# Kernel tuning notes

Measured on AMD Instinct MI355X. Metric: run time of the kernel, lower is better.

## Reference

```python
import jax, jax.numpy as jnp
import numpy as np

N, E, IN_C, HEADS, OUT_C = 50000, 800000, 256, 8, 32
NEG_SLOPE = 0.2
BN_EPS = 1e-5


def setup_inputs() -> dict:
    key = jax.random.key(0)
    ks = jax.random.split(key, 12)
    x = jax.random.normal(ks[0], (N, IN_C), jnp.float32)
    edge_index = jax.random.randint(ks[1], (2, E), 0, N, dtype=jnp.int32)
    edge_attr = jax.random.uniform(ks[2], (E, 1), jnp.float32)
    s = 0.1
    W = jax.random.normal(ks[3], (IN_C, HEADS * OUT_C), jnp.float32) * s
    att_src = jax.random.normal(ks[4], (HEADS, OUT_C), jnp.float32) * s
    att_dst = jax.random.normal(ks[5], (HEADS, OUT_C), jnp.float32) * s
    W_edge = jax.random.normal(ks[6], (1, HEADS * OUT_C), jnp.float32) * s
    att_edge = jax.random.normal(ks[7], (HEADS, OUT_C), jnp.float32) * s
    bias = jnp.zeros((HEADS * OUT_C,), jnp.float32)
    gamma = jnp.ones((HEADS * OUT_C,), jnp.float32)
    beta = jnp.zeros((HEADS * OUT_C,), jnp.float32)
    return {"x": x, "edge_index": edge_index, "edge_attr": edge_attr, "W": W,
            "att_src": att_src, "att_dst": att_dst, "W_edge": W_edge,
            "att_edge": att_edge, "bias": bias, "gamma": gamma, "beta": beta}


def reference(x, edge_index, edge_attr, W, att_src, att_dst, W_edge, att_edge, bias, gamma, beta):
    # --- add self loops (fill_value='mean' for edge_attr, PyG GATConv default) ---
    loops = jnp.arange(N, dtype=edge_index.dtype)
    src = jnp.concatenate([edge_index[0], loops])      # [E+N]
    dst = jnp.concatenate([edge_index[1], loops])      # [E+N]
    ea_mean = jnp.mean(edge_attr, axis=0, keepdims=True)
    ea = jnp.concatenate([edge_attr, jnp.broadcast_to(ea_mean, (N, edge_attr.shape[1]))], axis=0)

    # --- linear projections ---
    h = (x @ W).reshape(N, HEADS, OUT_C)               # [N,H,C]
    a_src = jnp.einsum('nhc,hc->nh', h, att_src)       # [N,H]
    a_dst = jnp.einsum('nhc,hc->nh', h, att_dst)       # [N,H]
    he = (ea @ W_edge).reshape(-1, HEADS, OUT_C)       # [E+N,H,C]
    a_edge = jnp.einsum('ehc,hc->eh', he, att_edge)    # [E+N,H]

    # --- edge-wise attention logits + segment softmax over destination nodes ---
    alpha = jax.nn.leaky_relu(a_src[src] + a_dst[dst] + a_edge, NEG_SLOPE)  # [E+N,H]
    amax = jax.ops.segment_max(alpha, dst, num_segments=N)  # every node has a self loop
    alpha = jnp.exp(alpha - amax[dst])
    asum = jax.ops.segment_sum(alpha, dst, num_segments=N)
    alpha = alpha / (asum[dst] + 1e-16)

    # --- weighted aggregation (attention dropout is identity in eval) ---
    msg = alpha[:, :, None] * h[src]                   # [E+N,H,C]
    out = jax.ops.segment_sum(msg, dst, num_segments=N).reshape(N, HEADS * OUT_C) + bias

    # --- BatchNorm (batch stats) + ELU; feature dropout is identity in eval ---
    mean = jnp.mean(out, axis=0)
    var = jnp.var(out, axis=0)
    out = (out - mean) * jax.lax.rsqrt(var + BN_EPS) * gamma + beta
    return jax.nn.elu(out)
```

## Files before the change

kernel.cpp:

```cpp
#include <hip/hip_runtime.h>
#include <hip/hip_bf16.h>
#include <math.h>

#define HEADS 8
#define OUTC 32
#define INC 256
#define OC 256
#define NEG_SLOPE 0.2f
#define BN_EPS 1e-5f
#define HS_STRIDE 264

typedef __attribute__((ext_vector_type(8))) short short8;
typedef __attribute__((ext_vector_type(4))) float floatx4;

__device__ __forceinline__ float bf2f(ushort u) {
    union { uint i; float f; } c; c.i = ((uint)u) << 16; return c.f;
}
__device__ __forceinline__ ushort f2bf(float f) {
    union { float f; uint i; } c; c.f = f;
    uint i = c.i + 0x7fffu + ((c.i >> 16) & 1u);
    return (ushort)(i >> 16);
}
__device__ __forceinline__ float loadf(const void* src, int t, uint flag) {
    return flag ? bf2f(((const ushort*)src)[t]) : ((const float*)src)[t];
}
__device__ __forceinline__ uint dtype_flag(const uint* gamma_raw) {
    return gamma_raw[0] != 0x3F800000u ? 1u : 0u;
}

__global__ void k_setup(const void* __restrict__ W, ushort* __restrict__ WT,
                        const void* __restrict__ att_src, const void* __restrict__ att_dst,
                        const void* __restrict__ gamma, const void* __restrict__ beta,
                        const void* __restrict__ We, const void* __restrict__ ae,
                        float* __restrict__ attS, float* __restrict__ attD,
                        float* __restrict__ gam, float* __restrict__ bet,
                        float* __restrict__ cvals, float* __restrict__ stats,
                        const void* __restrict__ eattr, const int* __restrict__ ei,
                        float* __restrict__ easum, int* __restrict__ deg, int E) {
    uint flag = dtype_flag((const uint*)gamma);
    int b = blockIdx.x, t = threadIdx.x;
    if (b < 256) {
        float v = loadf(W, b * OC + t, flag);
        WT[(size_t)t * INC + b] = f2bf(v);
    } else if (b == 256) {
        attS[t] = loadf(att_src, t, flag);
        attD[t] = loadf(att_dst, t, flag);
        gam[t]  = loadf(gamma, t, flag);
        bet[t]  = loadf(beta, t, flag);
        stats[t] = 0.f;
        stats[OC + t] = 0.f;
        __shared__ float s[OC];
        s[t] = loadf(We, t, flag) * loadf(ae, t, flag);
        __syncthreads();
        if (t < HEADS) {
            float v = 0.f;
            #pragma unroll
            for (int j = 0; j < OUTC; j++) v += s[t * OUTC + j];
            cvals[t] = v;
        }
    } else {
        int eb = b - 257;
        float v = 0.f;
        for (int i = eb * 256 + t; i < E; i += 512 * 256) {
            v += loadf(eattr, i, flag);
            atomicAdd(&deg[ei[E + i]], 1);
        }
        #pragma unroll
        for (int off = 32; off; off >>= 1) v += __shfl_down(v, off, 64);
        if ((t & 63) == 0) atomicAdd(easum, v);
    }
}

__global__ void __launch_bounds__(256, 2) k_gemm(const void* __restrict__ xraw,
                                                 const ushort* __restrict__ WT,
                                                 ushort* __restrict__ Hb,
                                                 const float* __restrict__ attS,
                                                 const float* __restrict__ attD,
                                                 float* __restrict__ asrc,
                                                 float* __restrict__ adst,
                                                 int N, const uint* __restrict__ graw) {
    uint flag = dtype_flag(graw);
    __shared__ ushort hs[16 * HS_STRIDE];
    int wave = threadIdx.x >> 6;
    int lane = threadIdx.x & 63;
    int m = lane & 15, q = lane >> 4;

    short8 bfr[4][8];
    #pragma unroll
    for (int i = 0; i < 4; i++) {
        const short8* wb = (const short8*)(WT + (size_t)((wave * 4 + i) * 16 + m) * INC);
        #pragma unroll
        for (int kk = 0; kk < 8; kk++) bfr[i][kk] = wb[kk * 4 + q];
    }

    int row0 = blockIdx.x << 4;
    #pragma unroll
    for (int c = 0; c < 2; c++) {
        int ch = threadIdx.x * 2 + c;
        int r = ch >> 5, seg = ch & 31;
        int row = row0 + r; if (row > N - 1) row = N - 1;
        short8 v;
        if (flag) {
            v = *(const short8*)((const ushort*)xraw + (size_t)row * INC + seg * 8);
        } else {
            const float4* xf = (const float4*)((const float*)xraw + (size_t)row * INC + seg * 8);
            float4 f0 = xf[0], f1 = xf[1];
            v[0] = (short)f2bf(f0.x); v[1] = (short)f2bf(f0.y);
            v[2] = (short)f2bf(f0.z); v[3] = (short)f2bf(f0.w);
            v[4] = (short)f2bf(f1.x); v[5] = (short)f2bf(f1.y);
            v[6] = (short)f2bf(f1.z); v[7] = (short)f2bf(f1.w);
        }
        *(short8*)(hs + r * HS_STRIDE + seg * 8) = v;
    }
    __syncthreads();
    short8 afr[8];
    #pragma unroll
    for (int kk = 0; kk < 8; kk++)
        afr[kk] = *(const short8*)(hs + m * HS_STRIDE + kk * 32 + q * 8);
    __syncthreads();
    floatx4 acc[4];
    #pragma unroll
    for (int i = 0; i < 4; i++) {
        floatx4 a = {0.f, 0.f, 0.f, 0.f};
        #pragma unroll
        for (int kk = 0; kk < 8; kk++)
            a = __builtin_amdgcn_mfma_f32_16x16x32_bf16(afr[kk], bfr[i][kk], a, 0, 0, 0);
        acc[i] = a;
    }
    #pragma unroll
    for (int i = 0; i < 4; i++) {
        int col = (wave * 4 + i) * 16 + m;
        #pragma unroll
        for (int r4 = 0; r4 < 4; r4++)
            hs[(q * 4 + r4) * HS_STRIDE + col] = f2bf(acc[i][r4]);
    }
    __syncthreads();
    #pragma unroll
    for (int c = 0; c < 2; c++) {
        int ch = threadIdx.x * 2 + c;
        int r = ch >> 5, seg = ch & 31;
        int row = row0 + r;
        if (row < N) {
            short8 v = *(const short8*)(hs + r * HS_STRIDE + seg * 8);
            *(short8*)(Hb + (size_t)row * OC + seg * 8) = v;
        }
    }
    if (threadIdx.x < 128) {
        int lr = threadIdx.x >> 3, hd = threadIdx.x & 7;
        int n = row0 + lr;
        if (n < N) {
            const ushort4* hrow = (const ushort4*)(hs + lr * HS_STRIDE + hd * OUTC);
            const float* as = attS + hd * OUTC;
            const float* ad = attD + hd * OUTC;
            float s1 = 0.f, s2 = 0.f;
            #pragma unroll
            for (int c4 = 0; c4 < 8; c4++) {
                ushort4 u = hrow[c4];
                float v0 = bf2f(u.x), v1 = bf2f(u.y), v2 = bf2f(u.z), v3 = bf2f(u.w);
                s1 += v0 * as[c4*4+0] + v1 * as[c4*4+1] + v2 * as[c4*4+2] + v3 * as[c4*4+3];
                s2 += v0 * ad[c4*4+0] + v1 * ad[c4*4+1] + v2 * ad[c4*4+2] + v3 * ad[c4*4+3];
            }
            asrc[n * HEADS + hd] = s1;
            adst[n * HEADS + hd] = s2;
        }
    }
}

__global__ void k_scan_local(const int* __restrict__ deg, int* __restrict__ part,
                             int* __restrict__ bsum, int N) {
    __shared__ int sth[256];
    int b = blockIdx.x, t = threadIdx.x;
    int base = b * 1024 + t * 4;
    int v0 = 0, v1 = 0, v2 = 0, v3 = 0;
    if (base + 0 < N) v0 = deg[base + 0] + 1;
    if (base + 1 < N) v1 = deg[base + 1] + 1;
    if (base + 2 < N) v2 = deg[base + 2] + 1;
    if (base + 3 < N) v3 = deg[base + 3] + 1;
    int tsum = v0 + v1 + v2 + v3;
    sth[t] = tsum;
    __syncthreads();
    #pragma unroll
    for (int off = 1; off < 256; off <<= 1) {
        int x = (t >= off) ? sth[t - off] : 0;
        __syncthreads();
        sth[t] += x;
        __syncthreads();
    }
    int excl = sth[t] - tsum;
    if (base + 0 < N) part[base + 0] = excl;
    if (base + 1 < N) part[base + 1] = excl + v0;
    if (base + 2 < N) part[base + 2] = excl + v0 + v1;
    if (base + 3 < N) part[base + 3] = excl + v0 + v1 + v2;
    if (t == 255) bsum[b] = sth[255];
}

__global__ void k_scan_blocks(const int* __restrict__ bsum, int* __restrict__ boff,
                              int nb, int* __restrict__ total) {
    __shared__ int sdata[256];
    __shared__ int carry;
    int t = threadIdx.x;
    if (t == 0) carry = 0;
    __syncthreads();
    for (int base = 0; base < nb; base += 256) {
        int v = (base + t < nb) ? bsum[base + t] : 0;
        sdata[t] = v;
        __syncthreads();
        #pragma unroll
        for (int off = 1; off < 256; off <<= 1) {
            int x = (t >= off) ? sdata[t - off] : 0;
            __syncthreads();
            sdata[t] += x;
            __syncthreads();
        }
        if (base + t < nb) boff[base + t] = carry + sdata[t] - v;
        __syncthreads();
        if (t == 255) carry += sdata[255];
        __syncthreads();
    }
    if (t == 0) total[0] = carry;
}

__global__ void k_scan_add(const int* __restrict__ part, const int* __restrict__ boff,
                           const int* __restrict__ total, int* __restrict__ rowstart,
                           int* __restrict__ cursor, int N) {
    int t = blockIdx.x * 256 + threadIdx.x;
    if (t < N) {
        int v = part[t] + boff[t >> 10];
        rowstart[t] = v;
        cursor[t]   = v;
    }
    if (t == 0) rowstart[N] = total[0];
}

__global__ void k_scatter(const int* __restrict__ ei, const void* __restrict__ eattr,
                          const float* __restrict__ easum, int* __restrict__ cursor,
                          uint* __restrict__ cpk, int E, int N,
                          const uint* __restrict__ graw) {
    uint flag = dtype_flag(graw);
    int t = blockIdx.x * 256 + threadIdx.x;
    if (t >= E + N) return;
    int s, d; float ea;
    if (t < E) { s = ei[t]; d = ei[E + t]; ea = loadf(eattr, t, flag); }
    else       { s = t - E; d = s;         ea = easum[0] / (float)E; }
    int pos = atomicAdd(&cursor[d], 1);
    cpk[pos] = ((uint)f2bf(ea) << 16) | ((uint)s & 0xFFFFu);
}

__global__ void __launch_bounds__(256) k_aggf(const int* __restrict__ rowstart,
                                              const uint* __restrict__ cpk,
                                              const float* __restrict__ asrc,
                                              const float* __restrict__ adst,
                                              const float* __restrict__ cvals,
                                              const ushort* __restrict__ Hb,
                                              ushort* __restrict__ outpre, int N) {
    int d = blockIdx.x * 4 + (threadIdx.x >> 6);
    if (d >= N) return;
    int lane = threadIdx.x & 63;
    int hd = lane >> 3;
    float ad = adst[d * HEADS + hd];
    float ch = cvals[hd];
    int beg = __builtin_amdgcn_readfirstlane(rowstart[d]);
    int end = __builtin_amdgcn_readfirstlane(rowstart[d + 1]);
    int l8 = lane & 7;
    float4 acc = {0.f, 0.f, 0.f, 0.f};
    float psum = 0.f;
    int j = beg;
    for (; j + 8 <= end; j += 8) {
        uint epack = cpk[j + l8];
        int sk[8]; float eaf[8];
        #pragma unroll
        for (int k = 0; k < 8; k++) {
            uint e = (uint)__builtin_amdgcn_readlane((int)epack, k);
            sk[k] = (int)(e & 0xFFFFu);
            eaf[k] = bf2f((ushort)(e >> 16));
        }
        ushort4 u[8]; float a[8];
        #pragma unroll
        for (int k = 0; k < 8; k++)
            u[k] = *(const ushort4*)(Hb + (size_t)sk[k] * OC + lane * 4);
        #pragma unroll
        for (int k = 0; k < 8; k++)
            a[k] = asrc[sk[k] * HEADS + hd];
        #pragma unroll
        for (int k = 0; k < 8; k++) {
            float l = (a[k] + ad) + eaf[k] * ch;
            l = fmaxf(l, NEG_SLOPE * l);
            float pe = __expf(l);
            psum += pe;
            acc.x += pe * bf2f(u[k].x); acc.y += pe * bf2f(u[k].y);
            acc.z += pe * bf2f(u[k].z); acc.w += pe * bf2f(u[k].w);
        }
    }
    int rem = end - j;
    if (rem > 0) {
        int jj = j + l8; if (jj > end - 1) jj = end - 1;
        uint epack = cpk[jj];
        int sk[8]; float eaf[8];
        #pragma unroll
        for (int k = 0; k < 8; k++) {
            uint e = (uint)__builtin_amdgcn_readlane((int)epack, k);
            sk[k] = (int)(e & 0xFFFFu);
            eaf[k] = bf2f((ushort)(e >> 16));
        }
        ushort4 u[8]; float a[8];
        #pragma unroll
        for (int k = 0; k < 8; k++)
            u[k] = *(const ushort4*)(Hb + (size_t)sk[k] * OC + lane * 4);
        #pragma unroll
        for (int k = 0; k < 8; k++)
            a[k] = asrc[sk[k] * HEADS + hd];
        #pragma unroll
        for (int k = 0; k < 8; k++) {
            float l = (a[k] + ad) + eaf[k] * ch;
            l = fmaxf(l, NEG_SLOPE * l);
            float pe = (k < rem) ? __expf(l) : 0.f;
            psum += pe;
            acc.x += pe * bf2f(u[k].x); acc.y += pe * bf2f(u[k].y);
            acc.z += pe * bf2f(u[k].z); acc.w += pe * bf2f(u[k].w);
        }
    }
    float inv = 1.f / (psum + 1e-16f);
    ushort4 o;
    o.x = f2bf(acc.x * inv); o.y = f2bf(acc.y * inv);
    o.z = f2bf(acc.z * inv); o.w = f2bf(acc.w * inv);
    *(ushort4*)(outpre + (size_t)d * OC + lane * 4) = o;
}

__global__ void __launch_bounds__(256) k_bnstats(const ushort* __restrict__ outpre,
                                                 float* __restrict__ stats, int N) {
    int t = threadIdx.x;
    int lane = t & 63, rr = t >> 6;
    int f4 = lane * 4;
    float r1[4] = {0.f, 0.f, 0.f, 0.f};
    float r2[4] = {0.f, 0.f, 0.f, 0.f};
    for (int n0 = blockIdx.x * 16 + rr * 4; n0 < N; n0 += gridDim.x * 16) {
        ushort4 u[4];
        #pragma unroll
        for (int j = 0; j < 4; j++) {
            int n = n0 + j;
            ushort4 z = {0, 0, 0, 0};
            u[j] = (n < N) ? *(const ushort4*)(outpre + (size_t)n * OC + f4) : z;
        }
        #pragma unroll
        for (int j = 0; j < 4; j++) {
            float v0 = bf2f(u[j].x), v1 = bf2f(u[j].y), v2 = bf2f(u[j].z), v3 = bf2f(u[j].w);
            r1[0] += v0; r2[0] += v0 * v0;
            r1[1] += v1; r2[1] += v1 * v1;
            r1[2] += v2; r2[2] += v2 * v2;
            r1[3] += v3; r2[3] += v3 * v3;
        }
    }
    __shared__ float sred[8][256];
    float4 a1 = {r1[0], r1[1], r1[2], r1[3]};
    float4 a2 = {r2[0], r2[1], r2[2], r2[3]};
    *(float4*)&sred[rr][f4]     = a1;
    *(float4*)&sred[4 + rr][f4] = a2;
    __syncthreads();
    float s1 = sred[0][t] + sred[1][t] + sred[2][t] + sred[3][t];
    float s2 = sred[4][t] + sred[5][t] + sred[6][t] + sred[7][t];
    atomicAdd(&stats[t], s1);
    atomicAdd(&stats[OC + t], s2);
}

__global__ void __launch_bounds__(256) k_bnelu(const ushort* __restrict__ outpre,
                                               const float* __restrict__ stats,
                                               const float* __restrict__ gam,
                                               const float* __restrict__ bet,
                                               void* __restrict__ out, int N,
                                               const uint* __restrict__ graw) {
    uint flag = dtype_flag(graw);
    __shared__ float sc[OC], sh[OC];
    int t = threadIdx.x;
    {
        float invN = 1.f / (float)N;
        float mean = stats[t] * invN;
        float var  = stats[OC + t] * invN - mean * mean;
        float s = rsqrtf(var + BN_EPS) * gam[t];
        sc[t] = s;
        sh[t] = bet[t] - mean * s;
    }
    __syncthreads();
    int lane = t & 63, rr = t >> 6;
    int f4 = lane * 4;
    float s0 = sc[f4 + 0], s1 = sc[f4 + 1], s2 = sc[f4 + 2], s3 = sc[f4 + 3];
    float h0 = sh[f4 + 0], h1 = sh[f4 + 1], h2 = sh[f4 + 2], h3 = sh[f4 + 3];
    for (int n = blockIdx.x * 4 + rr; n < N; n += gridDim.x * 4) {
        ushort4 u = *(const ushort4*)(outpre + (size_t)n * OC + f4);
        float r0 = bf2f(u.x) * s0 + h0;
        float r1 = bf2f(u.y) * s1 + h1;
        float r2 = bf2f(u.z) * s2 + h2;
        float r3 = bf2f(u.w) * s3 + h3;
        r0 = r0 > 0.f ? r0 : expm1f(r0);
        r1 = r1 > 0.f ? r1 : expm1f(r1);
        r2 = r2 > 0.f ? r2 : expm1f(r2);
        r3 = r3 > 0.f ? r3 : expm1f(r3);
        if (flag) {
            ushort4 o; o.x = f2bf(r0); o.y = f2bf(r1); o.z = f2bf(r2); o.w = f2bf(r3);
            *(ushort4*)((ushort*)out + (size_t)n * OC + f4) = o;
        } else {
            float4 o; o.x = r0; o.y = r1; o.z = r2; o.w = r3;
            *(float4*)((float*)out + (size_t)n * OC + f4) = o;
        }
    }
}

extern "C" void kernel_launch(void* const* d_in, const int* in_sizes, int n_in,
                              void* d_out, int out_size, void* d_ws, size_t ws_size,
                              hipStream_t stream) {
    const void* x        = d_in[0];
    const int*  ei       = (const int*)d_in[1];
    const void* eattr    = d_in[2];
    const void* W        = d_in[3];
    const void* att_src  = d_in[4];
    const void* att_dst  = d_in[5];
    const void* W_edge   = d_in[6];
    const void* att_edge = d_in[7];
    const void* gamma    = d_in[9];
    const void* beta     = d_in[10];
    const uint* graw     = (const uint*)gamma;

    int N = in_sizes[0] / INC;
    int E = in_sizes[1] / 2;
    int T = E + N;
    int nb = (N + 1023) / 1024;

    char* ws = (char*)d_ws;
    size_t off = 0;
    auto alloc = [&](size_t bytes) -> void* {
        void* pp = ws + off;
        off += (bytes + 255) & ~(size_t)255;
        return pp;
    };
    ushort* WT       = (ushort*)alloc((size_t)INC * OC * 2);
    float*  attS     = (float*)alloc(OC * 4);
    float*  attD     = (float*)alloc(OC * 4);
    float*  gam      = (float*)alloc(OC * 4);
    float*  bet      = (float*)alloc(OC * 4);
    ushort* Hb       = (ushort*)alloc((size_t)N * OC * 2);
    float*  asrc     = (float*)alloc((size_t)N * HEADS * 4);
    float*  adst     = (float*)alloc((size_t)N * HEADS * 4);
    int*    deg      = (int*)alloc((size_t)N * 4);
    int*    part     = (int*)alloc((size_t)N * 4);
    int*    bsum     = (int*)alloc((size_t)(nb + 1) * 4);
    int*    boff     = (int*)alloc((size_t)(nb + 1) * 4);
    int*    total    = (int*)alloc(256);
    int*    rowstart = (int*)alloc((size_t)(N + 1) * 4);
    int*    cursor   = (int*)alloc((size_t)N * 4);
    uint*   cpk      = (uint*)alloc((size_t)T * 4);
    ushort* outpre   = (ushort*)alloc((size_t)N * OC * 2);
    float*  stats    = (float*)alloc(2 * OC * 4);
    float*  easum    = (float*)alloc(256);
    float*  cvals    = (float*)alloc(256);

    hipMemsetAsync(easum, 0, 4, stream);
    hipMemsetAsync(deg, 0, (size_t)N * 4, stream);

    k_setup<<<769, 256, 0, stream>>>(W, WT, att_src, att_dst, gamma, beta, W_edge,
                                     att_edge, attS, attD, gam, bet, cvals, stats,
                                     eattr, ei, easum, deg, E);

    k_scan_local<<<nb, 256, 0, stream>>>(deg, part, bsum, N);
    k_scan_blocks<<<1, 256, 0, stream>>>(bsum, boff, nb, total);
    k_scan_add<<<(N + 255) / 256, 256, 0, stream>>>(part, boff, total, rowstart, cursor, N);
    k_scatter<<<(T + 255) / 256, 256, 0, stream>>>(ei, eattr, easum, cursor, cpk, E, N, graw);

    int tiles = (N + 15) / 16;
    k_gemm<<<tiles, 256, 0, stream>>>(x, WT, Hb, attS, attD, asrc, adst, N, graw);
    k_aggf<<<(N + 3) / 4, 256, 0, stream>>>(rowstart, cpk, asrc, adst, cvals, Hb, outpre, N);
    k_bnstats<<<512, 256, 0, stream>>>(outpre, stats, N);
    k_bnelu<<<512, 256, 0, stream>>>(outpre, stats, gam, bet, d_out, N, graw);
}
```

Before: 375.2 us.

## Make GEMM kernel persistent with double-buffered prefetch of next input tile

The projection GEMM now launches at most 1024 blocks, and each block loops over row tiles with a grid stride. This amortises the per-block load of the weight fragments into registers across several tiles. The next tile's x rows are loaded into registers while the MFMAs for the current tile run, then written to a second shared buffer. The output staging moves to its own shared array. Shared memory per block roughly triples and register pressure rises, which may reduce occupancy.

```diff
diff --git a/kernel.cpp b/kernel.cpp
--- a/kernel.cpp
+++ b/kernel.cpp
@@ -80,7 +80,8 @@
                                                  float* __restrict__ adst,
                                                  int N, const uint* __restrict__ graw) {
     uint flag = dtype_flag(graw);
-    __shared__ ushort hs[16 * HS_STRIDE];
+    __shared__ ushort hs[2][16 * HS_STRIDE];
+    __shared__ ushort hc[16 * HS_STRIDE];
     int wave = threadIdx.x >> 6;
     int lane = threadIdx.x & 63;
     int m = lane & 15, q = lane >> 4;
@@ -93,76 +94,107 @@
         for (int kk = 0; kk < 8; kk++) bfr[i][kk] = wb[kk * 4 + q];
     }
 
-    int row0 = blockIdx.x << 4;
-    #pragma unroll
-    for (int c = 0; c < 2; c++) {
-        int ch = threadIdx.x * 2 + c;
-        int r = ch >> 5, seg = ch & 31;
-        int row = row0 + r; if (row > N - 1) row = N - 1;
-        short8 v;
-        if (flag) {
-            v = *(const short8*)((const ushort*)xraw + (size_t)row * INC + seg * 8);
-        } else {
-            const float4* xf = (const float4*)((const float*)xraw + (size_t)row * INC + seg * 8);
-            float4 f0 = xf[0], f1 = xf[1];
-            v[0] = (short)f2bf(f0.x); v[1] = (short)f2bf(f0.y);
-            v[2] = (short)f2bf(f0.z); v[3] = (short)f2bf(f0.w);
-            v[4] = (short)f2bf(f1.x); v[5] = (short)f2bf(f1.y);
-            v[6] = (short)f2bf(f1.z); v[7] = (short)f2bf(f1.w);
-        }
-        *(short8*)(hs + r * HS_STRIDE + seg * 8) = v;
+    int ch0 = threadIdx.x * 2;
+    int r0c = ch0 >> 5, seg0 = ch0 & 31;
+    int r1c = (ch0 + 1) >> 5, seg1 = (ch0 + 1) & 31;
+
+    auto loadA = [&](int row0, short8& v0, short8& v1) {
+        #pragma unroll
+        for (int c = 0; c < 2; c++) {
+            int r = c ? r1c : r0c, seg = c ? seg1 : seg0;
+            int row = row0 + r; if (row > N - 1) row = N - 1;
+            short8 v;
+            if (flag) {
+                v = *(const short8*)((const ushort*)xraw + (size_t)row * INC + seg * 8);
+            } else {
+                const float4* xf = (const float4*)((const float*)xraw + (size_t)row * INC + seg * 8);
+                float4 f0 = xf[0], f1 = xf[1];
+                v[0] = (short)f2bf(f0.x); v[1] = (short)f2bf(f0.y);
+                v[2] = (short)f2bf(f0.z); v[3] = (short)f2bf(f0.w);
+                v[4] = (short)f2bf(f1.x); v[5] = (short)f2bf(f1.y);
+                v[6] = (short)f2bf(f1.z); v[7] = (short)f2bf(f1.w);
+            }
+            if (c == 0) v0 = v; else v1 = v;
+        }
+    };
+
+    int tiles = (N + 15) >> 4;
+    const int GRID = gridDim.x;
+    int rt = blockIdx.x;
+    if (rt >= tiles) return;
+
+    {
+        short8 v0, v1;
+        loadA(rt << 4, v0, v1);
+        *(short8*)(&hs[0][r0c * HS_STRIDE + seg0 * 8]) = v0;
+        *(short8*)(&hs[0][r1c * HS_STRIDE + seg1 * 8]) = v1;
     }
     __syncthreads();
-    short8 afr[8];
-    #pragma unroll
-    for (int kk = 0; kk < 8; kk++)
-        afr[kk] = *(const short8*)(hs + m * HS_STRIDE + kk * 32 + q * 8);
-    __syncthreads();
-    floatx4 acc[4];
-    #pragma unroll
-    for (int i = 0; i < 4; i++) {
-        floatx4 a = {0.f, 0.f, 0.f, 0.f};
+
+    int cur = 0;
+    while (true) {
+        int row0 = rt << 4;
+        int nrt = rt + GRID;
+        bool hasnext = nrt < tiles;
+        short8 nv0, nv1;
+        if (hasnext) loadA(nrt << 4, nv0, nv1);
+        short8 afr[8];
         #pragma unroll
         for (int kk = 0; kk < 8; kk++)
-            a = __builtin_amdgcn_mfma_f32_16x16x32_bf16(afr[kk], bfr[i][kk], a, 0, 0, 0);
-        acc[i] = a;
-    }
-    #pragma unroll
-    for (int i = 0; i < 4; i++) {
-        int col = (wave * 4 + i) * 16 + m;
-        #pragma unroll
-        for (int r4 = 0; r4 < 4; r4++)
-            hs[(q * 4 + r4) * HS_STRIDE + col] = f2bf(acc[i][r4]);
-    }
-    __syncthreads();
-    #pragma unroll
-    for (int c = 0; c < 2; c++) {
-        int ch = threadIdx.x * 2 + c;
-        int r = ch >> 5, seg = ch & 31;
-        int row = row0 + r;
-        if (row < N) {
-            short8 v = *(const short8*)(hs + r * HS_STRIDE + seg * 8);
-            *(short8*)(Hb + (size_t)row * OC + seg * 8) = v;
-        }
-    }
-    if (threadIdx.x < 128) {
-        int lr = threadIdx.x >> 3, hd = threadIdx.x & 7;
-        int n = row0 + lr;
-        if (n < N) {
-            const ushort4* hrow = (const ushort4*)(hs + lr * HS_STRIDE + hd * OUTC);
-            const float* as = attS + hd * OUTC;
-            const float* ad = attD + hd * OUTC;
-            float s1 = 0.f, s2 = 0.f;
+            afr[kk] = *(const short8*)(&hs[cur][m * HS_STRIDE + kk * 32 + q * 8]);
+        floatx4 acc[4];
+        #pragma unroll
+        for (int i = 0; i < 4; i++) {
+            floatx4 a = {0.f, 0.f, 0.f, 0.f};
             #pragma unroll
-            for (int c4 = 0; c4 < 8; c4++) {
-                ushort4 u = hrow[c4];
-                float v0 = bf2f(u.x), v1 = bf2f(u.y), v2 = bf2f(u.z), v3 = bf2f(u.w);
-                s1 += v0 * as[c4*4+0] + v1 * as[c4*4+1] + v2 * as[c4*4+2] + v3 * as[c4*4+3];
-                s2 += v0 * ad[c4*4+0] + v1 * ad[c4*4+1] + v2 * ad[c4*4+2] + v3 * ad[c4*4+3];
+            for (int kk = 0; kk < 8; kk++)
+                a = __builtin_amdgcn_mfma_f32_16x16x32_bf16(afr[kk], bfr[i][kk], a, 0, 0, 0);
+            acc[i] = a;
+        }
+        __syncthreads();
+        #pragma unroll
+        for (int i = 0; i < 4; i++) {
+            int col = (wave * 4 + i) * 16 + m;
+            #pragma unroll
+            for (int r4 = 0; r4 < 4; r4++)
+                hc[(q * 4 + r4) * HS_STRIDE + col] = f2bf(acc[i][r4]);
+        }
+        if (hasnext) {
+            *(short8*)(&hs[cur ^ 1][r0c * HS_STRIDE + seg0 * 8]) = nv0;
+            *(short8*)(&hs[cur ^ 1][r1c * HS_STRIDE + seg1 * 8]) = nv1;
+        }
+        __syncthreads();
+        #pragma unroll
+        for (int c = 0; c < 2; c++) {
+            int r = c ? r1c : r0c, seg = c ? seg1 : seg0;
+            int row = row0 + r;
+            if (row < N) {
+                short8 v = *(const short8*)(&hc[r * HS_STRIDE + seg * 8]);
+                *(short8*)(Hb + (size_t)row * OC + seg * 8) = v;
             }
-            asrc[n * HEADS + hd] = s1;
-            adst[n * HEADS + hd] = s2;
-        }
+        }
+        if (threadIdx.x < 128) {
+            int lr = threadIdx.x >> 3, hd = threadIdx.x & 7;
+            int n = row0 + lr;
+            if (n < N) {
+                const ushort4* hrow = (const ushort4*)(&hc[lr * HS_STRIDE + hd * OUTC]);
+                const float* as = attS + hd * OUTC;
+                const float* ad = attD + hd * OUTC;
+                float s1 = 0.f, s2 = 0.f;
+                #pragma unroll
+                for (int c4 = 0; c4 < 8; c4++) {
+                    ushort4 u = hrow[c4];
+                    float v0 = bf2f(u.x), v1 = bf2f(u.y), v2 = bf2f(u.z), v3 = bf2f(u.w);
+                    s1 += v0 * as[c4*4+0] + v1 * as[c4*4+1] + v2 * as[c4*4+2] + v3 * as[c4*4+3];
+                    s2 += v0 * ad[c4*4+0] + v1 * ad[c4*4+1] + v2 * ad[c4*4+2] + v3 * ad[c4*4+3];
+                }
+                asrc[n * HEADS + hd] = s1;
+                adst[n * HEADS + hd] = s2;
+            }
+        }
+        if (!hasnext) break;
+        rt = nrt;
+        cur ^= 1;
     }
 }
 
@@ -465,7 +497,8 @@
     k_scatter<<<(T + 255) / 256, 256, 0, stream>>>(ei, eattr, easum, cursor, cpk, E, N, graw);
 
     int tiles = (N + 15) / 16;
-    k_gemm<<<tiles, 256, 0, stream>>>(x, WT, Hb, attS, attD, asrc, adst, N, graw);
+    int gblocks = tiles < 1024 ? tiles : 1024;
+    k_gemm<<<gblocks, 256, 0, stream>>>(x, WT, Hb, attS, attD, asrc, adst, N, graw);
     k_aggf<<<(N + 3) / 4, 256, 0, stream>>>(rowstart, cpk, asrc, adst, cvals, Hb, outpre, N);
     k_bnstats<<<512, 256, 0, stream>>>(outpre, stats, N);
     k_bnelu<<<512, 256, 0, stream>>>(outpre, stats, gam, bet, d_out, N, graw);
```

After: 351.7 us. 6.3% less time.
